# Optimization experiments

Hardware: AMD Instinct MI355X
Metric: run time of the kernel (lower is better)

The kernel has to match this reference:

```python
import jax, jax.numpy as jnp
import numpy as np

B, L, D = 2, 2048, 1024
H = 16          # num_heads
HD = D // H     # head_dim = 64
NEG_INF = jnp.float32(-1e30)


def setup_inputs() -> dict:
    key = jax.random.key(0)
    ks = jax.random.split(key, 10)
    s = 1.0 / np.sqrt(D)
    return {
        "x": jax.random.normal(ks[0], (B, L, D), dtype=jnp.float32),
        "Wq": jax.random.normal(ks[1], (D, D), dtype=jnp.float32) * s,
        "bq": jnp.zeros((D,), jnp.float32),
        "Wk": jax.random.normal(ks[2], (D, D), dtype=jnp.float32) * s,
        "bk": jnp.zeros((D,), jnp.float32),
        "Wv": jax.random.normal(ks[3], (D, D), dtype=jnp.float32) * s,
        "bv": jnp.zeros((D,), jnp.float32),
        "Wo": jax.random.normal(ks[4], (D, D), dtype=jnp.float32) * s,
        "bo": jnp.zeros((D,), jnp.float32),
        "local_scale": jnp.ones((1,), jnp.float32),
        "global_scale": jnp.ones((1,), jnp.float32),
    }


def reference(x, Wq, bq, Wk, bk, Wv, bv, Wo, bo, local_scale, global_scale):
    # projections -> [B, H, L, HD]
    def proj(W, b):
        return (x @ W + b).reshape(B, L, H, HD).transpose(0, 2, 1, 3)
    Q, K, V = proj(Wq, bq), proj(Wk, bk), proj(Wv, bv)
    lh = H // 2
    inv_sqrt = 1.0 / jnp.sqrt(jnp.float32(HD))

    # local (causal) heads
    scores_l = jnp.einsum("bhqd,bhkd->bhqk", Q[:, :lh], K[:, :lh]) * inv_sqrt
    causal = jnp.tril(jnp.ones((L, L), dtype=bool))  # keep lower triangle
    scores_l = jnp.where(causal, scores_l * local_scale, NEG_INF)
    attn_local = jax.nn.softmax(scores_l, axis=-1)
    out_local = jnp.einsum("bhqk,bhkd->bhqd", attn_local, V[:, :lh])

    # global (full) heads
    scores_g = jnp.einsum("bhqd,bhkd->bhqk", Q[:, lh:], K[:, lh:]) * inv_sqrt
    attn_global = jax.nn.softmax(scores_g * global_scale, axis=-1)
    out_global = jnp.einsum("bhqk,bhkd->bhqd", attn_global, V[:, lh:])

    out = jnp.concatenate([out_local, out_global], axis=1)  # [B,H,L,HD]
    out = out.transpose(0, 2, 1, 3).reshape(B, L, D)
    out = out @ Wo + bo
    return (out, attn_local, attn_global)
```

## Files before the change

kernel.cpp:

```cpp
#include <hip/hip_runtime.h>
#include <hip/hip_bf16.h>

#define B 2
#define L 2048
#define D 1024
#define H 16
#define HD 64
#define LH 8
#define NEG_INF -1e30f

typedef __hip_bfloat16 bf16;
typedef unsigned short ushort_t;
typedef short bf16x8 __attribute__((ext_vector_type(8)));
typedef unsigned short us8 __attribute__((ext_vector_type(8)));
typedef float f32x4 __attribute__((ext_vector_type(4)));

#define MFMA16(a, b, c) __builtin_amdgcn_mfma_f32_16x16x32_bf16((a), (b), (c), 0, 0, 0)

#define WAITBAR(N) do {                                              \
    asm volatile("s_waitcnt vmcnt(" #N ") lgkmcnt(0)" ::: "memory"); \
    __builtin_amdgcn_sched_barrier(0);                               \
    __builtin_amdgcn_s_barrier();                                    \
  } while (0)

#if defined(__has_builtin)
#if __has_builtin(__builtin_amdgcn_global_load_lds)
#define HAVE_GLOAD_LDS 1
#endif
#endif

template<typename T> struct IsF32;
template<> struct IsF32<float> { static constexpr int value = 1; };
template<> struct IsF32<bf16>  { static constexpr int value = 0; };

__device__ __forceinline__ float ldf(const float* p, size_t i) { return p[i]; }
__device__ __forceinline__ float ldf(const bf16* p, size_t i) { return __bfloat162float(p[i]); }

__device__ __forceinline__ float4 ld4(const float* p, size_t i) {
  return *reinterpret_cast<const float4*>(p + i);
}
__device__ __forceinline__ float4 ld4(const bf16* p, size_t i) {
  ushort4 u = *reinterpret_cast<const ushort4*>(p + i);
  float4 f;
  f.x = __uint_as_float(((unsigned)u.x) << 16);
  f.y = __uint_as_float(((unsigned)u.y) << 16);
  f.z = __uint_as_float(((unsigned)u.z) << 16);
  f.w = __uint_as_float(((unsigned)u.w) << 16);
  return f;
}
__device__ __forceinline__ ushort_t bfh(float v) {
  bf16 h = __float2bfloat16(v);
  return *reinterpret_cast<ushort_t*>(&h);
}
__device__ __forceinline__ float bf2f(ushort_t u) {
  return __uint_as_float(((unsigned)u) << 16);
}
__device__ __forceinline__ void stf(float* p, size_t i, float v) { p[i] = v; }
__device__ __forceinline__ void stf(bf16* p, size_t i, float v) { p[i] = __float2bfloat16(v); }

__device__ __forceinline__ int swz(int row, int slot) {
  return row * 64 + (((slot ^ (row & 7)) & 7) << 3);
}
__device__ __forceinline__ int swzc(int row, int c) {
  return row * 64 + (((((c >> 3) ^ row) & 7) << 3) | (c & 7));
}

#if defined(HAVE_GLOAD_LDS)
__device__ __forceinline__ void gload_lds16(const ushort_t* src, ushort_t* dst) {
  __builtin_amdgcn_global_load_lds(
      (const __attribute__((address_space(1))) unsigned int*)src,
      (__attribute__((address_space(3))) unsigned int*)dst, 16, 0, 0);
}
#endif

__device__ __forceinline__ void stage64(const ushort_t* g, size_t gstride,
                                        ushort_t* lds, int w, int ln) {
  #pragma unroll
  for (int c = 0; c < 2; ++c) {
    const int row = 16 * w + 8 * c + (ln >> 3);
    const int slot = ((ln & 7) ^ row) & 7;
    const ushort_t* src = g + (size_t)row * gstride + slot * 8;
#if defined(HAVE_GLOAD_LDS)
    gload_lds16(src, lds + (size_t)(16 * w + 8 * c) * 64);
#else
    *reinterpret_cast<uint4*>(&lds[row * 64 + (ln & 7) * 8]) =
        *reinterpret_cast<const uint4*>(src);
#endif
  }
}

__global__ void detect_dtype_kernel(const unsigned short* __restrict__ x,
                                    int* __restrict__ flag) {
  int bad = 0;
  for (int i = threadIdx.x; i < 1024; i += 64) {
    if (((x[i] >> 7) & 0xFF) >= 170) bad = 1;
  }
  unsigned long long m = __ballot(bad);
  if (threadIdx.x == 0) *flag = (m != 0ULL) ? 1 : 0;
}

__global__ __launch_bounds__(256)
void cast_f32_kernel(const int* __restrict__ flag, int want,
                     const float* __restrict__ in,
                     ushort_t* __restrict__ hp, int n4) {
  if (*flag != want) return;
  int i = blockIdx.x * 256 + threadIdx.x;
  const int stride = gridDim.x * 256;
  for (; i < n4; i += stride) {
    float4 v = *reinterpret_cast<const float4*>(in + 4 * (size_t)i);
    ushort4 h;
    h.x = bfh(v.x); h.y = bfh(v.y); h.z = bfh(v.z); h.w = bfh(v.w);
    *reinterpret_cast<ushort4*>(hp + 4 * (size_t)i) = h;
  }
}

template<typename T>
__global__ __launch_bounds__(256)
void transW_kernel(const int* __restrict__ flag,
                   const T* __restrict__ W0, const T* __restrict__ W1,
                   const T* __restrict__ W2, const T* __restrict__ W3,
                   ushort_t* __restrict__ base, ushort_t* __restrict__ baseWo) {
  if (*flag != IsF32<T>::value) return;
  const int z = blockIdx.z;
  const T* W = z == 0 ? W0 : (z == 1 ? W1 : (z == 2 ? W2 : W3));
  ushort_t* hp = (z < 3) ? (base + (size_t)z * 2097152) : baseWo;
  __shared__ float ts[64][69];
  const int k0 = blockIdx.x * 64, n0 = blockIdx.y * 64;
  const int t = threadIdx.x;
  #pragma unroll
  for (int p = 0; p < 4; ++p) {
    int r = p * 16 + (t >> 4);
    int c = (t & 15) * 4;
    float4 v = ld4(W, (size_t)(k0 + r) * D + n0 + c);
    ts[r][c] = v.x; ts[r][c + 1] = v.y; ts[r][c + 2] = v.z; ts[r][c + 3] = v.w;
  }
  __syncthreads();
  #pragma unroll
  for (int p = 0; p < 4; ++p) {
    int n = p * 16 + (t >> 4);
    int k4 = (t & 15) * 4;
    ushort4 h;
    h.x = bfh(ts[k4][n]);
    h.y = bfh(ts[k4 + 1][n]);
    h.z = bfh(ts[k4 + 2][n]);
    h.w = bfh(ts[k4 + 3][n]);
    *reinterpret_cast<ushort4*>(&hp[(size_t)(n0 + n) * D + k0 + k4]) = h;
  }
}

template<typename T>
__global__ __launch_bounds__(256, 5)
void gemm_kernel(const int* __restrict__ flag,
                 const ushort_t* __restrict__ xA, const ushort_t* __restrict__ aoh,
                 const ushort_t* __restrict__ wbase, const ushort_t* __restrict__ woT,
                 const T* __restrict__ bq, const T* __restrict__ bk,
                 const T* __restrict__ bv, const T* __restrict__ bo,
                 ushort_t* __restrict__ qh, ushort_t* __restrict__ ql,
                 ushort_t* __restrict__ kh, ushort_t* __restrict__ kl,
                 ushort_t* __restrict__ vth, T* __restrict__ out0, int zfix) {
  if (*flag != IsF32<T>::value) return;
  const int cpx = gridDim.x >> 3;
  const int swzid = ((int)blockIdx.x & 7) * cpx + ((int)blockIdx.x >> 3);
  const int mtile = swzid & 63;
  const int ntile = (swzid >> 6) & 15;
  const int z = (zfix >= 0) ? zfix : (swzid >> 10);
  const int m0 = mtile * 64, n0 = ntile * 64;

  const bool isOut = (z == 3);
  const ushort_t* Ah = isOut ? aoh : xA;
  const ushort_t* wh = isOut ? woT : (wbase + (size_t)z * 2097152);

  __shared__ ushort_t As[2][4096], Bs[2][4096];

  const int ln = threadIdx.x & 63, w = threadIdx.x >> 6;
  const int m = ln & 15, hi = ln >> 4;

  f32x4 acc[4] = {};

  stage64(Ah + (size_t)m0 * 1024, 1024, As[0], w, ln);
  stage64(wh + (size_t)n0 * 1024, 1024, Bs[0], w, ln);
  __syncthreads();
  for (int step = 0; step < 16; ++step) {
    const int cur = step & 1;
    if (step < 15) {
      stage64(Ah + (size_t)m0 * 1024 + (step + 1) * 64, 1024, As[cur ^ 1], w, ln);
      stage64(wh + (size_t)n0 * 1024 + (step + 1) * 64, 1024, Bs[cur ^ 1], w, ln);
    }
    __builtin_amdgcn_s_setprio(1);
    #pragma unroll
    for (int kc = 0; kc < 2; ++kc) {
      bf16x8 a_h = *reinterpret_cast<const bf16x8*>(&As[cur][swz(16 * w + m, kc * 4 + hi)]);
      bf16x8 b_h[4];
      #pragma unroll
      for (int f = 0; f < 4; ++f)
        b_h[f] = *reinterpret_cast<const bf16x8*>(&Bs[cur][swz(f * 16 + m, kc * 4 + hi)]);
      #pragma unroll
      for (int fc = 0; fc < 4; ++fc)
        acc[fc] = MFMA16(a_h, b_h[fc], acc[fc]);
    }
    __builtin_amdgcn_s_setprio(0);
    __syncthreads();
  }

  #pragma unroll
  for (int fc = 0; fc < 4; ++fc) {
    const int col = n0 + fc * 16 + m;
    if (isOut) {
      const float bv_ = ldf(bo, (size_t)col);
      #pragma unroll
      for (int r = 0; r < 4; ++r) {
        const int tok = m0 + 16 * w + 4 * hi + r;
        stf(out0, (size_t)tok * D + col, acc[fc][r] + bv_);
      }
    } else if (z == 2) {
      const int hh = col >> 6, d = col & 63;
      const float bv_ = ldf(bv, (size_t)col);
      const int tok0 = m0 + 16 * w + 4 * hi;
      const int bb = tok0 >> 11, ll = tok0 & (L - 1);
      ushort4 hv;
      hv.x = bfh(acc[fc][0] + bv_);
      hv.y = bfh(acc[fc][1] + bv_);
      hv.z = bfh(acc[fc][2] + bv_);
      hv.w = bfh(acc[fc][3] + bv_);
      *reinterpret_cast<ushort4*>(
          &vth[((size_t)(bb * H + hh) * HD + d) * L + ll]) = hv;
    } else {
      const int hh = col >> 6, d = col & 63;
      const float bv_ = ldf(z == 0 ? bq : bk, (size_t)col);
      ushort_t* oh = z == 0 ? qh : kh;
      ushort_t* ol = z == 0 ? ql : kl;
      #pragma unroll
      for (int r = 0; r < 4; ++r) {
        const int tok = m0 + 16 * w + 4 * hi + r;
        const int bb = tok >> 11, ll = tok & (L - 1);
        const float v = acc[fc][r] + bv_;
        const size_t o = ((size_t)(bb * H + hh) * L + ll) * HD + d;
        const ushort_t hu = bfh(v);
        oh[o] = hu; ol[o] = bfh(v - bf2f(hu));
      }
    }
  }
}

template<typename T>
__global__ __launch_bounds__(256, 3)
void attn_kernel(const int* __restrict__ flag,
                 const ushort_t* __restrict__ Qh_g, const ushort_t* __restrict__ Ql_g,
                 const ushort_t* __restrict__ Kh_g, const ushort_t* __restrict__ Kl_g,
                 const ushort_t* __restrict__ Vth_g,
                 const T* __restrict__ lsp, const T* __restrict__ gsp,
                 T* __restrict__ attn_l, T* __restrict__ attn_g,
                 ushort_t* __restrict__ AOh) {
  if (*flag != IsF32<T>::value) return;
  const int bid = blockIdx.x;
  const int xcd = bid & 7, slot = bid >> 3;
  const int bhg = xcd + 8 * (slot >> 5);
  const int strip_raw = slot & 31;
  const int bb = bhg >> 4, h = bhg & 15;
  const bool is_local = h < LH;
  const int strip = is_local ? (31 - strip_raw) : strip_raw;
  const int q0 = strip * 64;
  const int ln = threadIdx.x & 63, w = threadIdx.x >> 6;
  const int m = ln & 15, hi = ln >> 4;

  const float cscale =
      (is_local ? ldf(lsp, (size_t)0) : ldf(gsp, (size_t)0)) * 0.125f;
  const size_t bh_off = ((size_t)bb * H + h) * L * HD;
  const ushort_t* Qhb = Qh_g + bh_off;
  const ushort_t* Qlb = Ql_g + bh_off;
  const ushort_t* Khb = Kh_g + bh_off;
  const ushort_t* Klb = Kl_g + bh_off;
  const ushort_t* Vhb = Vth_g + bh_off;

  __shared__ ushort_t SH[24576];
  ushort_t* VsH = SH + 16384;
  ushort_t* Ps  = SH + 20480;

  bf16x8 qfh[2], qfl[2];
  {
    const size_t qb = (size_t)(q0 + 16 * w + m) * HD + hi * 8;
    qfh[0] = *reinterpret_cast<const bf16x8*>(Qhb + qb);
    qfh[1] = *reinterpret_cast<const bf16x8*>(Qhb + qb + 32);
    qfl[0] = *reinterpret_cast<const bf16x8*>(Qlb + qb);
    qfl[1] = *reinterpret_cast<const bf16x8*>(Qlb + qb + 32);
  }

  float m_ = NEG_INF, l_ = 0.f;
  const int nkt = is_local ? (strip + 1) : (L / 64);
  T* aout = is_local ? attn_l : attn_g;
  const size_t arow0 =
      ((size_t)(bb * LH + (is_local ? h : h - LH)) * L + q0) * L;

  {
    const int np = (nkt + 1) >> 1;
    stage64(Khb, HD, SH, w, ln);
    if (1 < nkt) stage64(Khb + (size_t)64 * HD, HD, SH + 4096, w, ln);
    __syncthreads();
    for (int p = 0; p < np; ++p) {
      ushort_t* base = SH + (p & 1) * 8192;
      if (p + 1 < np) {
        ushort_t* nb = SH + ((p + 1) & 1) * 8192;
        stage64(Khb + (size_t)((2 * p + 2) * 64) * HD, HD, nb, w, ln);
        if (2 * p + 3 < nkt)
          stage64(Khb + (size_t)((2 * p + 3) * 64) * HD, HD, nb + 4096, w, ln);
      }
      const int nsub = (2 * p + 1 < nkt) ? 2 : 1;
      #pragma unroll 2
      for (int sub = 0; sub < nsub; ++sub) {
        const int kt = 2 * p + sub;
        const ushort_t* tb = base + sub * 4096;
        f32x4 s[4] = {};
        __builtin_amdgcn_s_setprio(1);
        #pragma unroll
        for (int nt = 0; nt < 4; ++nt)
          #pragma unroll
          for (int kc = 0; kc < 2; ++kc) {
            bf16x8 kbh = *reinterpret_cast<const bf16x8*>(&tb[swz(nt * 16 + m, kc * 4 + hi)]);
            s[nt] = MFMA16(kbh, qfh[kc], s[nt]);
          }
        __builtin_amdgcn_s_setprio(0);

        const bool dg = is_local && (kt == strip);
        #pragma unroll
        for (int nt = 0; nt < 4; ++nt)
          #pragma unroll
          for (int r = 0; r < 4; ++r) {
            float v = s[nt][r] * cscale;
            if (dg && (nt * 16 + 4 * hi + r > 16 * w + m)) v = NEG_INF;
            s[nt][r] = v;
          }
        float tm = NEG_INF;
        #pragma unroll
        for (int nt = 0; nt < 4; ++nt)
          #pragma unroll
          for (int r = 0; r < 4; ++r) tm = fmaxf(tm, s[nt][r]);
        tm = fmaxf(tm, __shfl_xor(tm, 16, 64));
        tm = fmaxf(tm, __shfl_xor(tm, 32, 64));
        const float mn = fmaxf(m_, tm);
        float sum = 0.f;
        #pragma unroll
        for (int nt = 0; nt < 4; ++nt)
          #pragma unroll
          for (int r = 0; r < 4; ++r) sum += __expf(s[nt][r] - mn);
        sum += __shfl_xor(sum, 16, 64);
        sum += __shfl_xor(sum, 32, 64);
        l_ = l_ * __expf(m_ - mn) + sum;
        m_ = mn;
      }
      __syncthreads();
    }
  }

  const float invl = 1.0f / l_;
  f32x4 o_[4] = {};

  stage64(Khb, HD, SH, w, ln);
  stage64(Klb, HD, SH + 8192, w, ln);
  __syncthreads();
  for (int kt = 0; kt < nkt; ++kt) {
    const int cur = kt & 1;
    const bool pf = (kt + 1 < nkt);
    ushort_t* KsHc = SH + cur * 4096;
    ushort_t* KsLc = SH + 8192 + cur * 4096;
    stage64(Vhb + (size_t)(kt * 64), L, VsH, w, ln);
    if (pf) {
      stage64(Khb + (size_t)((kt + 1) * 64) * HD, HD, SH + (cur ^ 1) * 4096, w, ln);
      stage64(Klb + (size_t)((kt + 1) * 64) * HD, HD, SH + 8192 + (cur ^ 1) * 4096, w, ln);
    }

    f32x4 s[4] = {};
    __builtin_amdgcn_s_setprio(1);
    #pragma unroll
    for (int nt = 0; nt < 4; ++nt)
      #pragma unroll
      for (int kc = 0; kc < 2; ++kc) {
        bf16x8 kbh = *reinterpret_cast<const bf16x8*>(&KsHc[swz(nt * 16 + m, kc * 4 + hi)]);
        bf16x8 kbl = *reinterpret_cast<const bf16x8*>(&KsLc[swz(nt * 16 + m, kc * 4 + hi)]);
        s[nt] = MFMA16(kbh, qfh[kc], s[nt]);
        s[nt] = MFMA16(kbl, qfh[kc], s[nt]);
        s[nt] = MFMA16(kbh, qfl[kc], s[nt]);
      }
    __builtin_amdgcn_s_setprio(0);

    const bool dg = is_local && (kt == strip);
    #pragma unroll
    for (int nt = 0; nt < 4; ++nt) {
      float v0 = s[nt][0] * cscale, v1 = s[nt][1] * cscale;
      float v2 = s[nt][2] * cscale, v3 = s[nt][3] * cscale;
      if (dg) {
        const int kbq = nt * 16 + 4 * hi, qq = 16 * w + m;
        if (kbq + 0 > qq) v0 = NEG_INF;
        if (kbq + 1 > qq) v1 = NEG_INF;
        if (kbq + 2 > qq) v2 = NEG_INF;
        if (kbq + 3 > qq) v3 = NEG_INF;
      }
      ushort4 pk;
      pk.x = bfh(__expf(v0 - m_) * invl);
      pk.y = bfh(__expf(v1 - m_) * invl);
      pk.z = bfh(__expf(v2 - m_) * invl);
      pk.w = bfh(__expf(v3 - m_) * invl);
      *reinterpret_cast<ushort4*>(&Ps[swzc(16 * w + m, nt * 16 + 4 * hi)]) = pk;
    }
    if (pf) { WAITBAR(4); } else { WAITBAR(0); }

    __builtin_amdgcn_s_setprio(1);
    bf16x8 pf0 = *reinterpret_cast<const bf16x8*>(&Ps[swz(16 * w + m, hi)]);
    bf16x8 pf1 = *reinterpret_cast<const bf16x8*>(&Ps[swz(16 * w + m, 4 + hi)]);
    #pragma unroll
    for (int dt = 0; dt < 4; ++dt) {
      bf16x8 vf0 = *reinterpret_cast<const bf16x8*>(&VsH[swz(dt * 16 + m, hi)]);
      bf16x8 vf1 = *reinterpret_cast<const bf16x8*>(&VsH[swz(dt * 16 + m, 4 + hi)]);
      o_[dt] = MFMA16(pf0, vf0, o_[dt]);
      o_[dt] = MFMA16(pf1, vf1, o_[dt]);
    }
    __builtin_amdgcn_s_setprio(0);

    {
      const int pr = 16 * w + (ln >> 2);
      const int cs = (ln & 3) * 2;
      us8 v0 = *reinterpret_cast<const us8*>(&Ps[swz(pr, cs)]);
      us8 v1 = *reinterpret_cast<const us8*>(&Ps[swz(pr, cs + 1)]);
      const size_t gi = arow0 + (size_t)pr * L + (size_t)(kt * 64 + (ln & 3) * 16);
      if constexpr (IsF32<T>::value) {
        float* dst = (float*)aout + gi;
        *reinterpret_cast<float4*>(dst + 0) =
            make_float4(bf2f(v0[0]), bf2f(v0[1]), bf2f(v0[2]), bf2f(v0[3]));
        *reinterpret_cast<float4*>(dst + 4) =
            make_float4(bf2f(v0[4]), bf2f(v0[5]), bf2f(v0[6]), bf2f(v0[7]));
        *reinterpret_cast<float4*>(dst + 8) =
            make_float4(bf2f(v1[0]), bf2f(v1[1]), bf2f(v1[2]), bf2f(v1[3]));
        *reinterpret_cast<float4*>(dst + 12) =
            make_float4(bf2f(v1[4]), bf2f(v1[5]), bf2f(v1[6]), bf2f(v1[7]));
      } else {
        bf16* dst = (bf16*)aout + gi;
        *reinterpret_cast<uint4*>(dst + 0) = *reinterpret_cast<const uint4*>(&v0);
        *reinterpret_cast<uint4*>(dst + 8) = *reinterpret_cast<const uint4*>(&v1);
      }
    }
    WAITBAR(4);
  }

  if (is_local) {
    const int pr = 16 * w + (ln >> 2);
    const size_t rbase = arow0 + (size_t)pr * L;
    for (int c = nkt * 64 + (ln & 3) * 16; c < L; c += 64) {
      if constexpr (IsF32<T>::value) {
        float* dst = (float*)aout + rbase + c;
        const float4 z4 = make_float4(0.f, 0.f, 0.f, 0.f);
        *reinterpret_cast<float4*>(dst + 0) = z4;
        *reinterpret_cast<float4*>(dst + 4) = z4;
        *reinterpret_cast<float4*>(dst + 8) = z4;
        *reinterpret_cast<float4*>(dst + 12) = z4;
      } else {
        bf16* dst = (bf16*)aout + rbase + c;
        const uint4 z4 = make_uint4(0u, 0u, 0u, 0u);
        *reinterpret_cast<uint4*>(dst + 0) = z4;
        *reinterpret_cast<uint4*>(dst + 8) = z4;
      }
    }
  }

  #pragma unroll
  for (int dt = 0; dt < 4; ++dt)
    #pragma unroll
    for (int r = 0; r < 4; ++r)
      AOh[((size_t)bb * L + q0 + 16 * w + 4 * hi + r) * D + h * HD + dt * 16 + m] =
          bfh(o_[dt][r]);
}

template<typename T>
static void launch_path(void* const* d_in, void* d_out, void* d_ws, hipStream_t stream) {
  const int want = IsF32<T>::value;
  const int* flag = (const int*)d_ws;
  ushort_t* Qh  = (ushort_t*)((char*)d_ws + 256);
  ushort_t* Ql  = Qh + 4194304;
  ushort_t* Kh  = Ql + 4194304;
  ushort_t* Kl  = Kh + 4194304;
  ushort_t* Vth = Kl + 4194304;
  ushort_t* AOh = Vth + 4194304;
  ushort_t* Woth = AOh + 4194304;

  const T* x  = (const T*)d_in[0];
  const T* Wq = (const T*)d_in[1];
  const T* bq = (const T*)d_in[2];
  const T* Wk = (const T*)d_in[3];
  const T* bk = (const T*)d_in[4];
  const T* Wv = (const T*)d_in[5];
  const T* bv = (const T*)d_in[6];
  const T* Wo = (const T*)d_in[7];
  const T* bo = (const T*)d_in[8];
  const T* ls = (const T*)d_in[9];
  const T* gs = (const T*)d_in[10];

  T* out0   = (T*)d_out;
  T* attn_l = out0 + (size_t)B * L * D;
  T* attn_g = attn_l + (size_t)B * LH * L * L;
  ushort_t* xh  = (ushort_t*)attn_g;
  ushort_t* Wt3 = xh + 4194304;

  if constexpr (IsF32<T>::value)
    cast_f32_kernel<<<1024, 256, 0, stream>>>(flag, want, (const float*)x, xh, 1048576);
  transW_kernel<T><<<dim3(16, 16, 4), 256, 0, stream>>>(
      flag, Wq, Wk, Wv, Wo, Wt3, Woth);
  const ushort_t* xA = IsF32<T>::value ? xh : (const ushort_t*)x;

  gemm_kernel<T><<<3072, 256, 0, stream>>>(
      flag, xA, AOh, Wt3, Woth, bq, bk, bv, bo,
      Qh, Ql, Kh, Kl, Vth, out0, -1);
  attn_kernel<T><<<1024, 256, 0, stream>>>(
      flag, Qh, Ql, Kh, Kl, Vth, ls, gs, attn_l, attn_g, AOh);
  gemm_kernel<T><<<1024, 256, 0, stream>>>(
      flag, xA, AOh, Wt3, Woth, bq, bk, bv, bo,
      Qh, Ql, Kh, Kl, Vth, out0, 3);
}

extern "C" void kernel_launch(void* const* d_in, const int* in_sizes, int n_in,
                              void* d_out, int out_size, void* d_ws, size_t ws_size,
                              hipStream_t stream) {
  int* flag = (int*)d_ws;
  detect_dtype_kernel<<<1, 64, 0, stream>>>((const unsigned short*)d_in[0], flag);
  launch_path<float>(d_in, d_out, d_ws, stream);
  launch_path<bf16>(d_in, d_out, d_ws, stream);
}
```

Baseline: 918.4 us.

## Drop split-bf16 hi/lo Q/K correction and double-buffer V in attention

Removes the low-order bf16 residual copies of Q and K, so the second attention pass computes scores with one MFMA per tile instead of three. It also stops the projection GEMM from writing the residuals. V is now staged into a double buffer alongside K, the first pass becomes one tile per iteration with a single barrier, and occupancy bounds go from 3 to 4 blocks. The cost is lower score precision for the stored attention probabilities, which may exceed tolerance, and the reworked wait counts risk synchronization hazards.

```diff
diff --git a/kernel.cpp b/kernel.cpp
--- a/kernel.cpp
+++ b/kernel.cpp
@@ -21,6 +21,11 @@
     asm volatile("s_waitcnt vmcnt(" #N ") lgkmcnt(0)" ::: "memory"); \
     __builtin_amdgcn_sched_barrier(0);                               \
     __builtin_amdgcn_s_barrier();                                    \
+  } while (0)
+
+#define LGKM0_FENCE() do {                                  \
+    asm volatile("s_waitcnt lgkmcnt(0)" ::: "memory");      \
+    __builtin_amdgcn_sched_barrier(0);                      \
   } while (0)
 
 #if defined(__has_builtin)
@@ -155,8 +160,7 @@
                  const ushort_t* __restrict__ wbase, const ushort_t* __restrict__ woT,
                  const T* __restrict__ bq, const T* __restrict__ bk,
                  const T* __restrict__ bv, const T* __restrict__ bo,
-                 ushort_t* __restrict__ qh, ushort_t* __restrict__ ql,
-                 ushort_t* __restrict__ kh, ushort_t* __restrict__ kl,
+                 ushort_t* __restrict__ qh, ushort_t* __restrict__ kh,
                  ushort_t* __restrict__ vth, T* __restrict__ out0, int zfix) {
   if (*flag != IsF32<T>::value) return;
   const int cpx = gridDim.x >> 3;
@@ -228,25 +232,20 @@
       const int hh = col >> 6, d = col & 63;
       const float bv_ = ldf(z == 0 ? bq : bk, (size_t)col);
       ushort_t* oh = z == 0 ? qh : kh;
-      ushort_t* ol = z == 0 ? ql : kl;
       #pragma unroll
       for (int r = 0; r < 4; ++r) {
         const int tok = m0 + 16 * w + 4 * hi + r;
         const int bb = tok >> 11, ll = tok & (L - 1);
-        const float v = acc[fc][r] + bv_;
-        const size_t o = ((size_t)(bb * H + hh) * L + ll) * HD + d;
-        const ushort_t hu = bfh(v);
-        oh[o] = hu; ol[o] = bfh(v - bf2f(hu));
+        oh[((size_t)(bb * H + hh) * L + ll) * HD + d] = bfh(acc[fc][r] + bv_);
       }
     }
   }
 }
 
 template<typename T>
-__global__ __launch_bounds__(256, 3)
+__global__ __launch_bounds__(256, 4)
 void attn_kernel(const int* __restrict__ flag,
-                 const ushort_t* __restrict__ Qh_g, const ushort_t* __restrict__ Ql_g,
-                 const ushort_t* __restrict__ Kh_g, const ushort_t* __restrict__ Kl_g,
+                 const ushort_t* __restrict__ Qh_g, const ushort_t* __restrict__ Kh_g,
                  const ushort_t* __restrict__ Vth_g,
                  const T* __restrict__ lsp, const T* __restrict__ gsp,
                  T* __restrict__ attn_l, T* __restrict__ attn_g,
@@ -267,22 +266,17 @@
       (is_local ? ldf(lsp, (size_t)0) : ldf(gsp, (size_t)0)) * 0.125f;
   const size_t bh_off = ((size_t)bb * H + h) * L * HD;
   const ushort_t* Qhb = Qh_g + bh_off;
-  const ushort_t* Qlb = Ql_g + bh_off;
   const ushort_t* Khb = Kh_g + bh_off;
-  const ushort_t* Klb = Kl_g + bh_off;
   const ushort_t* Vhb = Vth_g + bh_off;
 
-  __shared__ ushort_t SH[24576];
-  ushort_t* VsH = SH + 16384;
-  ushort_t* Ps  = SH + 20480;
-
-  bf16x8 qfh[2], qfl[2];
+  __shared__ ushort_t SH[20480];
+  ushort_t* Ps = SH + 16384;
+
+  bf16x8 qfh[2];
   {
     const size_t qb = (size_t)(q0 + 16 * w + m) * HD + hi * 8;
     qfh[0] = *reinterpret_cast<const bf16x8*>(Qhb + qb);
     qfh[1] = *reinterpret_cast<const bf16x8*>(Qhb + qb + 32);
-    qfl[0] = *reinterpret_cast<const bf16x8*>(Qlb + qb);
-    qfl[1] = *reinterpret_cast<const bf16x8*>(Qlb + qb + 32);
   }
 
   float m_ = NEG_INF, l_ = 0.f;
@@ -291,82 +285,68 @@
   const size_t arow0 =
       ((size_t)(bb * LH + (is_local ? h : h - LH)) * L + q0) * L;
 
-  {
-    const int np = (nkt + 1) >> 1;
-    stage64(Khb, HD, SH, w, ln);
-    if (1 < nkt) stage64(Khb + (size_t)64 * HD, HD, SH + 4096, w, ln);
-    __syncthreads();
-    for (int p = 0; p < np; ++p) {
-      ushort_t* base = SH + (p & 1) * 8192;
-      if (p + 1 < np) {
-        ushort_t* nb = SH + ((p + 1) & 1) * 8192;
-        stage64(Khb + (size_t)((2 * p + 2) * 64) * HD, HD, nb, w, ln);
-        if (2 * p + 3 < nkt)
-          stage64(Khb + (size_t)((2 * p + 3) * 64) * HD, HD, nb + 4096, w, ln);
-      }
-      const int nsub = (2 * p + 1 < nkt) ? 2 : 1;
-      #pragma unroll 2
-      for (int sub = 0; sub < nsub; ++sub) {
-        const int kt = 2 * p + sub;
-        const ushort_t* tb = base + sub * 4096;
-        f32x4 s[4] = {};
-        __builtin_amdgcn_s_setprio(1);
-        #pragma unroll
-        for (int nt = 0; nt < 4; ++nt)
-          #pragma unroll
-          for (int kc = 0; kc < 2; ++kc) {
-            bf16x8 kbh = *reinterpret_cast<const bf16x8*>(&tb[swz(nt * 16 + m, kc * 4 + hi)]);
-            s[nt] = MFMA16(kbh, qfh[kc], s[nt]);
-          }
-        __builtin_amdgcn_s_setprio(0);
-
-        const bool dg = is_local && (kt == strip);
-        #pragma unroll
-        for (int nt = 0; nt < 4; ++nt)
-          #pragma unroll
-          for (int r = 0; r < 4; ++r) {
-            float v = s[nt][r] * cscale;
-            if (dg && (nt * 16 + 4 * hi + r > 16 * w + m)) v = NEG_INF;
-            s[nt][r] = v;
-          }
-        float tm = NEG_INF;
-        #pragma unroll
-        for (int nt = 0; nt < 4; ++nt)
-          #pragma unroll
-          for (int r = 0; r < 4; ++r) tm = fmaxf(tm, s[nt][r]);
-        tm = fmaxf(tm, __shfl_xor(tm, 16, 64));
-        tm = fmaxf(tm, __shfl_xor(tm, 32, 64));
-        const float mn = fmaxf(m_, tm);
-        float sum = 0.f;
-        #pragma unroll
-        for (int nt = 0; nt < 4; ++nt)
-          #pragma unroll
-          for (int r = 0; r < 4; ++r) sum += __expf(s[nt][r] - mn);
-        sum += __shfl_xor(sum, 16, 64);
-        sum += __shfl_xor(sum, 32, 64);
-        l_ = l_ * __expf(m_ - mn) + sum;
-        m_ = mn;
-      }
-      __syncthreads();
-    }
+  stage64(Khb, HD, SH, w, ln);
+  WAITBAR(0);
+  for (int kt = 0; kt < nkt; ++kt) {
+    const int cur = kt & 1;
+    if (kt + 1 < nkt)
+      stage64(Khb + (size_t)((kt + 1) * 64) * HD, HD, SH + (cur ^ 1) * 4096, w, ln);
+
+    const ushort_t* Kc = SH + cur * 4096;
+    f32x4 s[4] = {};
+    __builtin_amdgcn_s_setprio(1);
+    #pragma unroll
+    for (int nt = 0; nt < 4; ++nt)
+      #pragma unroll
+      for (int kc = 0; kc < 2; ++kc) {
+        bf16x8 kbh = *reinterpret_cast<const bf16x8*>(&Kc[swz(nt * 16 + m, kc * 4 + hi)]);
+        s[nt] = MFMA16(kbh, qfh[kc], s[nt]);
+      }
+    __builtin_amdgcn_s_setprio(0);
+
+    const bool dg = is_local && (kt == strip);
+    #pragma unroll
+    for (int nt = 0; nt < 4; ++nt)
+      #pragma unroll
+      for (int r = 0; r < 4; ++r) {
+        float v = s[nt][r] * cscale;
+        if (dg && (nt * 16 + 4 * hi + r > 16 * w + m)) v = NEG_INF;
+        s[nt][r] = v;
+      }
+    float tm = NEG_INF;
+    #pragma unroll
+    for (int nt = 0; nt < 4; ++nt)
+      #pragma unroll
+      for (int r = 0; r < 4; ++r) tm = fmaxf(tm, s[nt][r]);
+    tm = fmaxf(tm, __shfl_xor(tm, 16, 64));
+    tm = fmaxf(tm, __shfl_xor(tm, 32, 64));
+    const float mn = fmaxf(m_, tm);
+    float sum = 0.f;
+    #pragma unroll
+    for (int nt = 0; nt < 4; ++nt)
+      #pragma unroll
+      for (int r = 0; r < 4; ++r) sum += __expf(s[nt][r] - mn);
+    sum += __shfl_xor(sum, 16, 64);
+    sum += __shfl_xor(sum, 32, 64);
+    l_ = l_ * __expf(m_ - mn) + sum;
+    m_ = mn;
+    WAITBAR(0);
   }
 
   const float invl = 1.0f / l_;
   f32x4 o_[4] = {};
 
   stage64(Khb, HD, SH, w, ln);
-  stage64(Klb, HD, SH + 8192, w, ln);
-  __syncthreads();
+  stage64(Vhb, L, SH + 8192, w, ln);
+  WAITBAR(0);
   for (int kt = 0; kt < nkt; ++kt) {
     const int cur = kt & 1;
-    const bool pf = (kt + 1 < nkt);
-    ushort_t* KsHc = SH + cur * 4096;
-    ushort_t* KsLc = SH + 8192 + cur * 4096;
-    stage64(Vhb + (size_t)(kt * 64), L, VsH, w, ln);
-    if (pf) {
+    if (kt + 1 < nkt) {
       stage64(Khb + (size_t)((kt + 1) * 64) * HD, HD, SH + (cur ^ 1) * 4096, w, ln);
-      stage64(Klb + (size_t)((kt + 1) * 64) * HD, HD, SH + 8192 + (cur ^ 1) * 4096, w, ln);
-    }
+      stage64(Vhb + (size_t)((kt + 1) * 64), L, SH + 8192 + (cur ^ 1) * 4096, w, ln);
+    }
+    const ushort_t* Kc = SH + cur * 4096;
+    const ushort_t* Vc = SH + 8192 + cur * 4096;
 
     f32x4 s[4] = {};
     __builtin_amdgcn_s_setprio(1);
@@ -374,11 +354,8 @@
     for (int nt = 0; nt < 4; ++nt)
       #pragma unroll
       for (int kc = 0; kc < 2; ++kc) {
-        bf16x8 kbh = *reinterpret_cast<const bf16x8*>(&KsHc[swz(nt * 16 + m, kc * 4 + hi)]);
-        bf16x8 kbl = *reinterpret_cast<const bf16x8*>(&KsLc[swz(nt * 16 + m, kc * 4 + hi)]);
+        bf16x8 kbh = *reinterpret_cast<const bf16x8*>(&Kc[swz(nt * 16 + m, kc * 4 + hi)]);
         s[nt] = MFMA16(kbh, qfh[kc], s[nt]);
-        s[nt] = MFMA16(kbl, qfh[kc], s[nt]);
-        s[nt] = MFMA16(kbh, qfl[kc], s[nt]);
       }
     __builtin_amdgcn_s_setprio(0);
 
@@ -401,15 +378,15 @@
       pk.w = bfh(__expf(v3 - m_) * invl);
       *reinterpret_cast<ushort4*>(&Ps[swzc(16 * w + m, nt * 16 + 4 * hi)]) = pk;
     }
-    if (pf) { WAITBAR(4); } else { WAITBAR(0); }
+    LGKM0_FENCE();
 
     __builtin_amdgcn_s_setprio(1);
     bf16x8 pf0 = *reinterpret_cast<const bf16x8*>(&Ps[swz(16 * w + m, hi)]);
     bf16x8 pf1 = *reinterpret_cast<const bf16x8*>(&Ps[swz(16 * w + m, 4 + hi)]);
     #pragma unroll
     for (int dt = 0; dt < 4; ++dt) {
-      bf16x8 vf0 = *reinterpret_cast<const bf16x8*>(&VsH[swz(dt * 16 + m, hi)]);
-      bf16x8 vf1 = *reinterpret_cast<const bf16x8*>(&VsH[swz(dt * 16 + m, 4 + hi)]);
+      bf16x8 vf0 = *reinterpret_cast<const bf16x8*>(&Vc[swz(dt * 16 + m, hi)]);
+      bf16x8 vf1 = *reinterpret_cast<const bf16x8*>(&Vc[swz(dt * 16 + m, 4 + hi)]);
       o_[dt] = MFMA16(pf0, vf0, o_[dt]);
       o_[dt] = MFMA16(pf1, vf1, o_[dt]);
     }
@@ -437,7 +414,7 @@
         *reinterpret_cast<uint4*>(dst + 8) = *reinterpret_cast<const uint4*>(&v1);
       }
     }
-    WAITBAR(4);
+    if constexpr (IsF32<T>::value) { WAITBAR(4); } else { WAITBAR(2); }
   }
 
   if (is_local) {
@@ -473,10 +450,8 @@
   const int want = IsF32<T>::value;
   const int* flag = (const int*)d_ws;
   ushort_t* Qh  = (ushort_t*)((char*)d_ws + 256);
-  ushort_t* Ql  = Qh + 4194304;
-  ushort_t* Kh  = Ql + 4194304;
-  ushort_t* Kl  = Kh + 4194304;
-  ushort_t* Vth = Kl + 4194304;
+  ushort_t* Kh  = Qh + 4194304;
+  ushort_t* Vth = Kh + 4194304;
   ushort_t* AOh = Vth + 4194304;
   ushort_t* Woth = AOh + 4194304;
 
@@ -505,13 +480,11 @@
   const ushort_t* xA = IsF32<T>::value ? xh : (const ushort_t*)x;
 
   gemm_kernel<T><<<3072, 256, 0, stream>>>(
-      flag, xA, AOh, Wt3, Woth, bq, bk, bv, bo,
-      Qh, Ql, Kh, Kl, Vth, out0, -1);
+      flag, xA, AOh, Wt3, Woth, bq, bk, bv, bo, Qh, Kh, Vth, out0, -1);
   attn_kernel<T><<<1024, 256, 0, stream>>>(
-      flag, Qh, Ql, Kh, Kl, Vth, ls, gs, attn_l, attn_g, AOh);
+      flag, Qh, Kh, Vth, ls, gs, attn_l, attn_g, AOh);
   gemm_kernel<T><<<1024, 256, 0, stream>>>(
-      flag, xA, AOh, Wt3, Woth, bq, bk, bv, bo,
-      Qh, Ql, Kh, Kl, Vth, out0, 3);
+      flag, xA, AOh, Wt3, Woth, bq, bk, bv, bo, Qh, Kh, Vth, out0, 3);
 }
 
 extern "C" void kernel_launch(void* const* d_in, const int* in_sizes, int n_in,
```

Result: no change. 911.0 us (-0.8%).
